# Kernel tuning notes

Hardware: AMD Instinct MI355X
Metric: run time of the kernel (lower is better)

Reference implementation:

```python
import jax, jax.numpy as jnp
import numpy as np
import math

IN_FEATURES = 64
OUT_FEATURES = 64
GRID_SIZE = 17
GRID_RANGE = 2.5
BATCH = 8192


def setup_inputs() -> dict:
    key = jax.random.key(0)
    k1, k2, k3 = jax.random.split(key, 3)
    fan = 1.0 / math.sqrt(float(IN_FEATURES))
    inputs = jax.random.normal(k1, (BATCH, IN_FEATURES), dtype=jnp.float32)
    base_scale = jax.random.normal(k2, (IN_FEATURES, OUT_FEATURES), dtype=jnp.float32) * fan
    spline_weight = jax.random.normal(k3, (IN_FEATURES, OUT_FEATURES, GRID_SIZE), dtype=jnp.float32) * (0.1 * fan)
    output_bias = jnp.zeros((OUT_FEATURES,), dtype=jnp.float32)
    return {"inputs": inputs, "base_scale": base_scale, "spline_weight": spline_weight, "output_bias": output_bias}


def reference(inputs, base_scale, spline_weight, output_bias):
    # grid buffer: linspace over [-grid_range, grid_range]
    grid = jnp.linspace(-GRID_RANGE, GRID_RANGE, GRID_SIZE, dtype=jnp.float32)
    spacing = grid[1] - grid[0]
    # degree-1 B-spline (hat) basis: [B, in, grid]
    basis = jnp.maximum(1.0 - jnp.abs(inputs[..., None] - grid) / spacing, 0.0)
    # per-edge spline output: [B, in, out]
    spline_output = jnp.einsum('big,iog->bio', basis, spline_weight)
    # SiLU residual path, per edge
    base_output = jax.nn.silu(inputs)[..., None] * base_scale[None, :, :]
    edge_output = base_output + spline_output
    # sum incoming edges per destination node, normalized
    output = edge_output.sum(axis=1) / math.sqrt(float(IN_FEATURES)) + output_bias
    # dropout=0.0 -> identity
    return (output, edge_output, basis)
```

## Files before the change

### kernel.cpp

```cpp
#include <hip/hip_runtime.h>
#include <math.h>

#define NBATCH 8192
#define NIN 64
#define NOUT 64
#define NG 17

typedef float f32x4 __attribute__((ext_vector_type(4)));

#define OUT_ELEMS   (NBATCH * NOUT)
#define EDGE_ELEMS  (NBATCH * NIN * NOUT)
#define WT_FLOATS   (NIN * NG * NOUT)
#define WT_BYTES    (WT_FLOATS * sizeof(float))

__global__ void kan_transpose_w(const float* __restrict__ W, float* __restrict__ Wt) {
    int idx = blockIdx.x * blockDim.x + threadIdx.x;
    if (idx >= NIN * NOUT * NG) return;
    int i   = idx / (NOUT * NG);
    int rem = idx - i * (NOUT * NG);
    int o   = rem / NG;
    int g   = rem - o * NG;
    Wt[(i * NG + g) * NOUT + o] = W[idx];
}

__global__ __launch_bounds__(512) void kan_kernel(
    const float* __restrict__ x,
    const float* __restrict__ scale,
    const float* __restrict__ Wt,
    const float* __restrict__ bias,
    float* __restrict__ out,
    float* __restrict__ edge,
    float* __restrict__ basis)
{
    const int tid  = threadIdx.x;
    const int wave = tid >> 6;
    const int lane = tid & 63;
    const int b = blockIdx.x * 8 + wave;

    __shared__ float s_scale[NIN * NOUT];
    __shared__ float s_silu[8][64];
    __shared__ float s_t[8][64];
    __shared__ int   s_g0[8][64];

    {
        const f32x4* s4 = (const f32x4*)scale;
        f32x4* d4 = (f32x4*)s_scale;
        d4[tid]       = s4[tid];
        d4[tid + 512] = s4[tid + 512];
    }

    {
        float xv  = x[b * NIN + lane];
        float sig = 1.0f / (1.0f + __expf(-xv));
        s_silu[wave][lane] = xv * sig;
        float u   = (xv + 2.5f) * 3.2f;
        float g0f = floorf(u);
        s_t[wave][lane]  = u - g0f;
        s_g0[wave][lane] = (int)g0f;
    }
    __syncthreads();

    {
        float* brow = basis + (size_t)b * (NIN * NG);
        #pragma unroll
        for (int k = 0; k < 4; ++k) {
            int p0 = (k * 64 + lane) * 4;
            f32x4 v;
            #pragma unroll
            for (int e = 0; e < 4; ++e) {
                int p = p0 + e;
                int i = (int)((unsigned)p / 17u);
                int g = p - i * 17;
                int   g0 = s_g0[wave][i];
                float t  = s_t[wave][i];
                v[e] = (g == g0) ? (1.0f - t) : ((g == g0 + 1) ? t : 0.0f);
            }
            *(f32x4*)(brow + p0) = v;
        }
        if (lane < 16) {
            int p0 = (256 + lane) * 4;
            f32x4 v;
            #pragma unroll
            for (int e = 0; e < 4; ++e) {
                int p = p0 + e;
                int i = (int)((unsigned)p / 17u);
                int g = p - i * 17;
                int   g0 = s_g0[wave][i];
                float t  = s_t[wave][i];
                v[e] = (g == g0) ? (1.0f - t) : ((g == g0 + 1) ? t : 0.0f);
            }
            *(f32x4*)(brow + p0) = v;
        }
    }

    f32x4 acc = {0.f, 0.f, 0.f, 0.f};
    float* erow = edge + (size_t)b * (NIN * NOUT);
    const int iq = lane >> 4;
    const int o  = (lane & 15) * 4;
    #pragma unroll 4
    for (int ib = 0; ib < NIN; ib += 4) {
        int   i  = ib + iq;
        float sl = s_silu[wave][i];
        float t  = s_t[wave][i];
        int   g0 = s_g0[wave][i];
        f32x4 sc = *(const f32x4*)(s_scale + i * NOUT + o);
        f32x4 w0 = {0.f, 0.f, 0.f, 0.f};
        f32x4 w1 = {0.f, 0.f, 0.f, 0.f};
        if ((unsigned)g0       < (unsigned)NG) w0 = *(const f32x4*)(Wt + (i * NG + g0)     * NOUT + o);
        if ((unsigned)(g0 + 1) < (unsigned)NG) w1 = *(const f32x4*)(Wt + (i * NG + g0 + 1) * NOUT + o);
        float mt = 1.0f - t;
        f32x4 v = sl * sc + mt * w0 + t * w1;
        *(f32x4*)(erow + i * NOUT + o) = v;
        acc += v;
    }
    #pragma unroll
    for (int e = 0; e < 4; ++e) {
        float a = acc[e];
        a += __shfl_xor(a, 16);
        a += __shfl_xor(a, 32);
        acc[e] = a;
    }
    if (lane < 16) {
        f32x4 bi = *(const f32x4*)(bias + lane * 4);
        f32x4 r = acc * 0.125f + bi;
        *(f32x4*)(out + (size_t)b * NOUT + lane * 4) = r;
    }
}

extern "C" void kernel_launch(void* const* d_in, const int* in_sizes, int n_in,
                              void* d_out, int out_size, void* d_ws, size_t ws_size,
                              hipStream_t stream) {
    const float* x     = (const float*)d_in[0];
    const float* scale = (const float*)d_in[1];
    const float* W     = (const float*)d_in[2];
    const float* bias  = (const float*)d_in[3];

    float* out   = (float*)d_out;
    float* edge  = out + OUT_ELEMS;
    float* basis = edge + EDGE_ELEMS;

    float* Wt = (float*)d_ws;
    const int n = NIN * NOUT * NG;
    if (ws_size >= WT_BYTES) {
        kan_transpose_w<<<(n + 255) / 256, 256, 0, stream>>>(W, Wt);
        kan_kernel<<<dim3(NBATCH / 8), dim3(512), 0, stream>>>(x, scale, Wt, bias, out, edge, basis);
    }
}
```

Baseline: 39.27 us.

## Stage spline weights and scale as bf16 in shared memory, drop transpose kernel

Removes the separate weight transpose kernel. Each block now transposes the spline weights and base scale itself, rounding them to bf16 and staging them in dynamic shared memory (about 150 KB). Blocks process 32 batch rows instead of 8, which amortizes the staging, and per-input metadata is packed into one float4 with clamped grid indices so the weight loads need no branches. Truncating weights to bf16 introduces precision loss in edge_output and output, and every block re-reads W from global memory in a strided pattern.

```diff
diff --git a/kernel.cpp b/kernel.cpp
--- a/kernel.cpp
+++ b/kernel.cpp
@@ -10,120 +10,137 @@
 
 #define OUT_ELEMS   (NBATCH * NOUT)
 #define EDGE_ELEMS  (NBATCH * NIN * NOUT)
-#define WT_FLOATS   (NIN * NG * NOUT)
-#define WT_BYTES    (WT_FLOATS * sizeof(float))
 
-__global__ void kan_transpose_w(const float* __restrict__ W, float* __restrict__ Wt) {
-    int idx = blockIdx.x * blockDim.x + threadIdx.x;
-    if (idx >= NIN * NOUT * NG) return;
-    int i   = idx / (NOUT * NG);
-    int rem = idx - i * (NOUT * NG);
-    int o   = rem / NG;
-    int g   = rem - o * NG;
-    Wt[(i * NG + g) * NOUT + o] = W[idx];
+#define WT_U16      (NIN * NG * NOUT)
+#define SC_U16      (NIN * NOUT)
+#define SHMEM_BYTES ((WT_U16 + SC_U16) * 2)
+
+__device__ __forceinline__ f32x4 bf4_to_f4(ushort4 h) {
+    f32x4 f;
+    f.x = __uint_as_float(((unsigned)h.x) << 16);
+    f.y = __uint_as_float(((unsigned)h.y) << 16);
+    f.z = __uint_as_float(((unsigned)h.z) << 16);
+    f.w = __uint_as_float(((unsigned)h.w) << 16);
+    return f;
 }
 
 __global__ __launch_bounds__(512) void kan_kernel(
     const float* __restrict__ x,
     const float* __restrict__ scale,
-    const float* __restrict__ Wt,
+    const float* __restrict__ W,
     const float* __restrict__ bias,
     float* __restrict__ out,
     float* __restrict__ edge,
     float* __restrict__ basis)
 {
+    extern __shared__ unsigned short s_dyn[];
+    unsigned short* s_wt = s_dyn;
+    unsigned short* s_sc = s_dyn + WT_U16;
+    __shared__ f32x4 s_meta[8][64];
+
     const int tid  = threadIdx.x;
     const int wave = tid >> 6;
     const int lane = tid & 63;
-    const int b = blockIdx.x * 8 + wave;
+    const int row0 = blockIdx.x * 32;
 
-    __shared__ float s_scale[NIN * NOUT];
-    __shared__ float s_silu[8][64];
-    __shared__ float s_t[8][64];
-    __shared__ int   s_g0[8][64];
+    float xr[4];
+    #pragma unroll
+    for (int r = 0; r < 4; ++r)
+        xr[r] = x[(row0 + r * 8 + wave) * NIN + lane];
+    f32x4 bi4 = *(const f32x4*)(bias + (lane & 15) * 4);
 
-    {
-        const f32x4* s4 = (const f32x4*)scale;
-        f32x4* d4 = (f32x4*)s_scale;
-        d4[tid]       = s4[tid];
-        d4[tid + 512] = s4[tid + 512];
+    for (int p = tid; p < WT_U16 / 2; p += 512) {
+        int o2  = p & 31;
+        int rem = p >> 5;
+        int g   = rem % 17;
+        int i   = rem / 17;
+        int gb  = (i * NOUT + o2 * 2) * NG + g;
+        unsigned lo = __float_as_uint(W[gb])      >> 16;
+        unsigned hi = __float_as_uint(W[gb + NG]) >> 16;
+        ((unsigned*)s_wt)[p] = lo | (hi << 16);
     }
-
-    {
-        float xv  = x[b * NIN + lane];
-        float sig = 1.0f / (1.0f + __expf(-xv));
-        s_silu[wave][lane] = xv * sig;
-        float u   = (xv + 2.5f) * 3.2f;
-        float g0f = floorf(u);
-        s_t[wave][lane]  = u - g0f;
-        s_g0[wave][lane] = (int)g0f;
+    for (int p = tid; p < SC_U16 / 2; p += 512) {
+        unsigned lo = __float_as_uint(scale[2 * p])     >> 16;
+        unsigned hi = __float_as_uint(scale[2 * p + 1]) >> 16;
+        ((unsigned*)s_sc)[p] = lo | (hi << 16);
     }
     __syncthreads();
 
-    {
-        float* brow = basis + (size_t)b * (NIN * NG);
+    for (int r = 0; r < 4; ++r) {
+        const int b = row0 + r * 8 + wave;
+
+        {
+            float xv  = xr[r];
+            float sig = 1.0f / (1.0f + __expf(-xv));
+            float sl  = xv * sig;
+            float u   = (xv + 2.5f) * 3.2f;
+            float g0f = floorf(u);
+            float t   = u - g0f;
+            int   g0  = (int)g0f;
+            float tw0 = ((unsigned)g0       < 17u) ? (1.0f - t) : 0.0f;
+            float tw1 = ((unsigned)(g0 + 1) < 17u) ? t          : 0.0f;
+            int g0c = min(max(g0, 0), 16);
+            int g1c = min(max(g0 + 1, 0), 16);
+            f32x4 m;
+            m.x = sl; m.y = tw0; m.z = tw1;
+            m.w = __uint_as_float((unsigned)g0c | ((unsigned)g1c << 16));
+            s_meta[wave][lane] = m;
+        }
+
+        {
+            float* brow = basis + (size_t)b * (NIN * NG);
+            #pragma unroll
+            for (int k = 0; k < 5; ++k) {
+                int f4 = k * 64 + lane;
+                if (f4 < 272) {
+                    int p0 = f4 * 4;
+                    f32x4 v;
+                    #pragma unroll
+                    for (int e = 0; e < 4; ++e) {
+                        int p = p0 + e;
+                        int i = (int)((unsigned)p / 17u);
+                        int g = p - i * 17;
+                        f32x4 m = s_meta[wave][i];
+                        unsigned gg = __float_as_uint(m.w);
+                        int g0c = (int)(gg & 0xffffu);
+                        int g1c = (int)(gg >> 16);
+                        v[e] = ((g == g0c) ? m.y : 0.0f) + ((g == g1c) ? m.z : 0.0f);
+                    }
+                    *(f32x4*)(brow + p0) = v;
+                }
+            }
+        }
+
+        f32x4 acc = {0.f, 0.f, 0.f, 0.f};
+        float* erow = edge + (size_t)b * (NIN * NOUT);
+        const int iq   = lane >> 4;
+        const int ocol = (lane & 15) * 4;
+        #pragma unroll 4
+        for (int ib = 0; ib < NIN; ib += 4) {
+            int i = ib + iq;
+            f32x4 m = s_meta[wave][i];
+            unsigned gg = __float_as_uint(m.w);
+            int g0c = (int)(gg & 0xffffu);
+            int g1c = (int)(gg >> 16);
+            const unsigned short* wbase = s_wt + i * (NG * NOUT) + ocol;
+            f32x4 w0 = bf4_to_f4(*(const ushort4*)(wbase + g0c * NOUT));
+            f32x4 w1 = bf4_to_f4(*(const ushort4*)(wbase + g1c * NOUT));
+            f32x4 sc = bf4_to_f4(*(const ushort4*)(s_sc + i * NOUT + ocol));
+            f32x4 v = m.x * sc + m.y * w0 + m.z * w1;
+            *(f32x4*)(erow + ib * NOUT + lane * 4) = v;
+            acc += v;
+        }
         #pragma unroll
-        for (int k = 0; k < 4; ++k) {
-            int p0 = (k * 64 + lane) * 4;
-            f32x4 v;
-            #pragma unroll
-            for (int e = 0; e < 4; ++e) {
-                int p = p0 + e;
-                int i = (int)((unsigned)p / 17u);
-                int g = p - i * 17;
-                int   g0 = s_g0[wave][i];
-                float t  = s_t[wave][i];
-                v[e] = (g == g0) ? (1.0f - t) : ((g == g0 + 1) ? t : 0.0f);
-            }
-            *(f32x4*)(brow + p0) = v;
+        for (int e = 0; e < 4; ++e) {
+            float a = acc[e];
+            a += __shfl_xor(a, 16);
+            a += __shfl_xor(a, 32);
+            acc[e] = a;
         }
         if (lane < 16) {
-            int p0 = (256 + lane) * 4;
-            f32x4 v;
-            #pragma unroll
-            for (int e = 0; e < 4; ++e) {
-                int p = p0 + e;
-                int i = (int)((unsigned)p / 17u);
-                int g = p - i * 17;
-                int   g0 = s_g0[wave][i];
-                float t  = s_t[wave][i];
-                v[e] = (g == g0) ? (1.0f - t) : ((g == g0 + 1) ? t : 0.0f);
-            }
-            *(f32x4*)(brow + p0) = v;
+            f32x4 rr = acc * 0.125f + bi4;
+            *(f32x4*)(out + (size_t)b * NOUT + lane * 4) = rr;
         }
-    }
-
-    f32x4 acc = {0.f, 0.f, 0.f, 0.f};
-    float* erow = edge + (size_t)b * (NIN * NOUT);
-    const int iq = lane >> 4;
-    const int o  = (lane & 15) * 4;
-    #pragma unroll 4
-    for (int ib = 0; ib < NIN; ib += 4) {
-        int   i  = ib + iq;
-        float sl = s_silu[wave][i];
-        float t  = s_t[wave][i];
-        int   g0 = s_g0[wave][i];
-        f32x4 sc = *(const f32x4*)(s_scale + i * NOUT + o);
-        f32x4 w0 = {0.f, 0.f, 0.f, 0.f};
-        f32x4 w1 = {0.f, 0.f, 0.f, 0.f};
-        if ((unsigned)g0       < (unsigned)NG) w0 = *(const f32x4*)(Wt + (i * NG + g0)     * NOUT + o);
-        if ((unsigned)(g0 + 1) < (unsigned)NG) w1 = *(const f32x4*)(Wt + (i * NG + g0 + 1) * NOUT + o);
-        float mt = 1.0f - t;
-        f32x4 v = sl * sc + mt * w0 + t * w1;
-        *(f32x4*)(erow + i * NOUT + o) = v;
-        acc += v;
-    }
-    #pragma unroll
-    for (int e = 0; e < 4; ++e) {
-        float a = acc[e];
-        a += __shfl_xor(a, 16);
-        a += __shfl_xor(a, 32);
-        acc[e] = a;
-    }
-    if (lane < 16) {
-        f32x4 bi = *(const f32x4*)(bias + lane * 4);
-        f32x4 r = acc * 0.125f + bi;
-        *(f32x4*)(out + (size_t)b * NOUT + lane * 4) = r;
     }
 }
 
@@ -139,10 +156,6 @@
     float* edge  = out + OUT_ELEMS;
     float* basis = edge + EDGE_ELEMS;
 
-    float* Wt = (float*)d_ws;
-    const int n = NIN * NOUT * NG;
-    if (ws_size >= WT_BYTES) {
-        kan_transpose_w<<<(n + 255) / 256, 256, 0, stream>>>(W, Wt);
-        kan_kernel<<<dim3(NBATCH / 8), dim3(512), 0, stream>>>(x, scale, Wt, bias, out, edge, basis);
-    }
+    kan_kernel<<<dim3(256), dim3(512), SHMEM_BYTES, stream>>>(
+        x, scale, W, bias, out, edge, basis);
 }
```

Result: slower. 49.02 us (+24.8%).
